# Performance work log

Measured on AMD Instinct MI355X. Metric: run time of the kernel, lower is better.

## Reference

```python
import jax, jax.numpy as jnp
import numpy as np

N, E, W_IN, W_OUT, NUM_CLASS, M = 4096, 5, 512, 128, 16, 1024
NUM_LAYERS, ALPHA, THETA = 64, 0.1, 0.5

def leaky_relu(x):
    return jnp.where(x >= 0, x, 0.01 * x)

def setup_inputs() -> dict:
    key = jax.random.key(0)
    ks = jax.random.split(key, 16)
    u = jax.random.uniform(ks[0], (N, N, E), jnp.float32)
    A = jnp.where(u < 0.01, u, 0.0)
    X = jax.random.normal(ks[1], (N, W_IN), jnp.float32)
    target_x = jax.random.randint(ks[2], (M,), 0, N)
    target = jax.random.randint(ks[3], (M,), 0, NUM_CLASS)
    def xav(k, shape):
        fan_in, fan_out = shape[-2], shape[-1]
        lim = (6.0 / (fan_in + fan_out)) ** 0.5
        return jax.random.uniform(k, shape, jnp.float32, -lim, lim)
    H0 = W_IN + E * W_OUT  # DGCN input width
    return dict(
        A=A, X=X, target_x=target_x, target=target,
        weight=xav(ks[4], (W_IN, W_OUT)),
        attw=xav(ks[5], (1, N)),
        attb=jnp.zeros((1, W_OUT), jnp.float32),
        attq=xav(ks[6], (1, W_OUT)),
        Wg=xav(ks[7], (W_IN, W_IN)), bg=jnp.zeros((W_IN,), jnp.float32),
        W0=xav(ks[8], (H0, W_OUT)), b0=jnp.zeros((W_OUT,), jnp.float32),
        Wconvs=xav(ks[9], (NUM_LAYERS, W_OUT, W_OUT)),
        Wd1=xav(ks[10], (W_OUT, W_OUT)), bd1=jnp.zeros((W_OUT,), jnp.float32),
        W1=xav(ks[11], (W_OUT, W_OUT)), b1=jnp.zeros((W_OUT,), jnp.float32),
        W2=xav(ks[12], (W_OUT, NUM_CLASS)), b2=jnp.zeros((NUM_CLASS,), jnp.float32),
    )

def reference(A, X, target_x, target, weight, attw, attb, attq, Wg, bg, W0, b0,
              Wconvs, Wd1, bd1, W1, b1, W2, b2):
    Ae = jnp.transpose(A, (2, 0, 1))              # [E,N,N]
    I = jnp.eye(N, dtype=A.dtype)
    # gcn_conv feature transform is identical for every edge type (dropout p=0)
    Xw = leaky_relu(leaky_relu(X @ Wg + bg) @ weight)   # [N, w_out]
    # norm(H, add=True): transpose, set diagonal to 1, row-normalize by degree
    Ht = Ae.transpose(0, 2, 1) * (1.0 - I) + I          # [E,N,N]
    deg = Ht.sum(-1)
    dinv = jnp.where(deg > 0, 1.0 / deg, 0.0)
    lgcn = jax.nn.relu(jnp.einsum('enm,md->end', dinv[..., None] * Ht, Xw))  # [E,N,w_out]
    # edge-type attention
    tm = jnp.tanh(jnp.einsum('n,end->ed', attw[0], lgcn) + attb)  # [E,w_out]
    watt = (tm * attq[0]).sum(-1)                                  # [E]
    beta = jax.nn.softmax(watt) * E
    Xcat = (beta[:, None, None] * lgcn).transpose(1, 0, 2).reshape(N, E * W_OUT)
    X_ = jnp.concatenate([Xcat, X], axis=1)       # [N, w_in + E*w_out]
    # DGCN: GCNII stack on binary nonzero pattern of mean adjacency, gcn_norm
    B = (jnp.mean(Ae, 0) != 0).astype(A.dtype)
    Bs = jnp.maximum(B, I)                        # add remaining self-loops
    d = Bs.sum(1)
    dis = jnp.where(d > 0, jax.lax.rsqrt(d), 0.0)
    A_hat = dis[:, None] * Bs * dis[None, :]      # D^-1/2 (B+I) D^-1/2
    x0 = jax.nn.relu(X_ @ W0 + b0)                # [N, w_out]
    betas_l = jnp.log(THETA / jnp.arange(1, NUM_LAYERS + 1, dtype=A.dtype) + 1.0)
    def step(x, inp):
        Wl, bl = inp
        h = A_hat @ x
        h = (1.0 - ALPHA) * h + ALPHA * x0        # initial residual
        x = jax.nn.relu((1.0 - bl) * h + bl * (h @ Wl))  # identity mapping
        return x, None
    x, _ = jax.lax.scan(step, x0, (Wconvs, betas_l))
    Z = leaky_relu(x @ Wd1 + bd1)                 # DGCN lins[1] + outer leaky_relu
    Z = leaky_relu(Z @ W1 + b1)                   # linear1
    y = Z[target_x] @ W2 + b2                     # linear2 on labeled nodes [M,C]
    logp = jax.nn.log_softmax(y, axis=-1)
    loss = -jnp.mean(jnp.take_along_axis(logp, target[:, None], axis=1))
    return loss, y
```

## Files before the change

### kernel.cpp

```cpp
#include <hip/hip_runtime.h>
#include <cstdint>
#include <cmath>

#define NN   4096
#define EE   5
#define WIN  512
#define WOUT 128
#define HH0  1152
#define NLAY 64
#define NCLS 16
#define MT   1024
#define GCAP 96
#define BCAP 320
#define ECAP 48
#define KSPLIT 16
#define KCHUNK 256

typedef __attribute__((ext_vector_type(8))) short     bf16x8_t;
typedef __attribute__((ext_vector_type(8))) unsigned short ushort8_t;
typedef __attribute__((ext_vector_type(4))) float     f32x4_t;

__device__ inline unsigned short f2bf(float f) {
  unsigned int u = __float_as_uint(f);
  unsigned int r = (u + 0x7FFFu + ((u >> 16) & 1u)) >> 16;
  return (unsigned short)r;
}

__device__ __forceinline__ void gload16(const unsigned short* g, unsigned short* l) {
  __builtin_amdgcn_global_load_lds(
      (__attribute__((address_space(1))) void*)g,
      (__attribute__((address_space(3))) void*)l, 16, 0, 0);
}

__global__ __launch_bounds__(256) void gemm_kernel(
    const float* __restrict__ A, const float* __restrict__ W,
    const float* __restrict__ bias, float* __restrict__ C,
    int Mdim, int Kdim, int Ndim, int act) {
  __shared__ __align__(16) float sA[16][68];
  __shared__ __align__(16) float sW[16][64];
  int tid = threadIdx.x;
  int tx = tid & 15, ty = tid >> 4;
  int row0 = blockIdx.y * 64, col0 = blockIdx.x * 64;
  float acc[4][4] = {};
  int mA = tid >> 2;
  int kA = (tid & 3) << 2;
  int kW = tid >> 4;
  int nW = (tid & 15) << 2;
  for (int k0 = 0; k0 < Kdim; k0 += 16) {
    float4 av = *(const float4*)(A + (size_t)(row0 + mA) * Kdim + k0 + kA);
    float4 wv = *(const float4*)(W + (size_t)(k0 + kW) * Ndim + col0 + nW);
    sA[kA + 0][mA] = av.x;
    sA[kA + 1][mA] = av.y;
    sA[kA + 2][mA] = av.z;
    sA[kA + 3][mA] = av.w;
    *(float4*)&sW[kW][nW] = wv;
    __syncthreads();
#pragma unroll
    for (int kk = 0; kk < 16; kk++) {
      float4 a = *(const float4*)&sA[kk][ty << 2];
      float4 b = *(const float4*)&sW[kk][tx << 2];
      acc[0][0] += a.x * b.x; acc[0][1] += a.x * b.y; acc[0][2] += a.x * b.z; acc[0][3] += a.x * b.w;
      acc[1][0] += a.y * b.x; acc[1][1] += a.y * b.y; acc[1][2] += a.y * b.z; acc[1][3] += a.y * b.w;
      acc[2][0] += a.z * b.x; acc[2][1] += a.z * b.y; acc[2][2] += a.z * b.z; acc[2][3] += a.z * b.w;
      acc[3][0] += a.w * b.x; acc[3][1] += a.w * b.y; acc[3][2] += a.w * b.z; acc[3][3] += a.w * b.w;
    }
    __syncthreads();
  }
#pragma unroll
  for (int i = 0; i < 4; i++) {
    int r = row0 + (ty << 2) + i;
#pragma unroll
    for (int jc = 0; jc < 4; jc++) {
      int c = col0 + (tx << 2) + jc;
      float o = acc[i][jc];
      if (bias) o += bias[c];
      if (act == 1) o = fmaxf(o, 0.f);
      else if (act == 2) o = (o >= 0.f) ? o : 0.01f * o;
      C[(size_t)r * Ndim + c] = o;
    }
  }
}

__global__ __launch_bounds__(256) void scan_rows_kernel(
    const float* __restrict__ A, int* __restrict__ fcnt, int* __restrict__ fidx,
    float* __restrict__ fval, int* __restrict__ bcnt, int* __restrict__ bidx) {
  __shared__ int   lbuf[1024];
  __shared__ int   lcnt;
  __shared__ int   ecnt[EE];
  __shared__ int   en2[EE][ECAP];
  __shared__ float ev[EE][ECAP];
  __shared__ int   rbase;
  __shared__ int   gbase[EE];
  int tid = threadIdx.x;
  int n1 = blockIdx.x >> 2;
  int qb = (blockIdx.x & 3) << 10;
  if (tid == 0) lcnt = 0;
  if (tid < EE) ecnt[tid] = 0;
  __syncthreads();
  const float4* src = (const float4*)(A + ((size_t)n1 * NN + qb) * EE);
  float buf[20];
  float4* bf4 = (float4*)buf;
#pragma unroll
  for (int c = 0; c < 5; c++) bf4[c] = src[tid * 5 + c];
  int n2base = qb + tid * 4;
#pragma unroll
  for (int u = 0; u < 4; u++) {
    int n2 = n2base + u;
    if (n2 == n1) continue;
    bool any = false;
#pragma unroll
    for (int e = 0; e < EE; e++) {
      float v = buf[u * 5 + e];
      if (v != 0.f) {
        any = true;
        int s = atomicAdd(&ecnt[e], 1);
        if (s < ECAP) { en2[e][s] = n2; ev[e][s] = v; }
      }
    }
    if (any) {
      int s = atomicAdd(&lcnt, 1);
      lbuf[s] = n2;
    }
  }
  __syncthreads();
  if (tid == 0) rbase = atomicAdd(&bcnt[n1], lcnt);
  if (tid < EE) gbase[tid] = atomicAdd(&fcnt[tid * NN + n1], min(ecnt[tid], ECAP));
  __syncthreads();
  int c = lcnt, rb = rbase;
  for (int s = tid; s < c; s += 256)
    if (rb + s < BCAP) bidx[(size_t)n1 * BCAP + rb + s] = lbuf[s];
#pragma unroll
  for (int e = 0; e < EE; e++) {
    int ec = min(ecnt[e], ECAP), gb = gbase[e];
    size_t base = ((size_t)e * NN + n1) * GCAP;
    for (int s = tid; s < ec; s += 256) {
      if (gb + s < GCAP) {
        fidx[base + gb + s] = en2[e][s];
        fval[base + gb + s] = ev[e][s];
      }
    }
  }
}

__global__ __launch_bounds__(64) void transpose_kernel(
    const int* __restrict__ fcnt, const int* __restrict__ fidx, const float* __restrict__ fval,
    int* __restrict__ gcnt, int* __restrict__ gidx, float* __restrict__ gval) {
  int id = blockIdx.x;
  int n1 = id & (NN - 1);
  int e  = id >> 12;
  int c = min(fcnt[id], GCAP);
  for (int s = threadIdx.x; s < c; s += 64) {
    int   n2 = fidx[(size_t)id * GCAP + s];
    float v  = fval[(size_t)id * GCAP + s];
    int t = e * NN + n2;
    int slot = atomicAdd(&gcnt[t], 1);
    if (slot < GCAP) {
      gidx[(size_t)t * GCAP + slot] = n1;
      gval[(size_t)t * GCAP + slot] = v;
    }
  }
}

__global__ void dinv_dis_kernel(const int* __restrict__ gcnt, const float* __restrict__ gval,
                                float* __restrict__ dinv, const int* __restrict__ bcnt,
                                float* __restrict__ dis) {
  int t = blockIdx.x * 256 + threadIdx.x;
  if (t < EE * NN) {
    int cnt = min(gcnt[t], GCAP);
    float s = 1.0f;
    for (int k = 0; k < cnt; k++) s += gval[(size_t)t * GCAP + k];
    dinv[t] = 1.0f / s;
  }
  if (t < NN) dis[t] = rsqrtf(1.0f + (float)min(bcnt[t], BCAP));
}

__global__ __launch_bounds__(256) void build_ahat_kernel(
    const int* __restrict__ bcnt, const int* __restrict__ bidx,
    const float* __restrict__ dis, unsigned short* __restrict__ Ab) {
  __shared__ unsigned int bits[128];
  int i = blockIdx.x, t = threadIdx.x;
  if (t < 128) bits[t] = 0;
  __syncthreads();
  int cnt = min(bcnt[i], BCAP);
  for (int s = t; s < cnt; s += 256) {
    int j = bidx[(size_t)i * BCAP + s];
    atomicOr(&bits[j >> 5], 1u << (j & 31));
  }
  __syncthreads();
  float di = dis[i];
  int c0 = t * 16;
  unsigned short out[16];
#pragma unroll
  for (int u = 0; u < 16; u++) {
    int j = c0 + u;
    bool on = ((bits[j >> 5] >> (j & 31)) & 1u) || (j == i);
    out[u] = on ? f2bf(di * dis[j]) : (unsigned short)0;
  }
  *(ushort8_t*)&Ab[(size_t)i * NN + c0]     = *(ushort8_t*)&out[0];
  *(ushort8_t*)&Ab[(size_t)i * NN + c0 + 8] = *(ushort8_t*)&out[8];
}

__global__ __launch_bounds__(128) void lgcn_kernel(
    const int* __restrict__ gcnt, const int* __restrict__ gidx, const float* __restrict__ gval,
    const float* __restrict__ dinv, const float* __restrict__ Xw, float* __restrict__ lgcn) {
  int i = blockIdx.x, e = blockIdx.y, d = threadIdx.x;
  int t = e * NN + i;
  int cnt = min(gcnt[t], GCAP);
  __shared__ int   sj[GCAP];
  __shared__ float sv[GCAP];
  for (int s = d; s < cnt; s += 128) {
    sj[s] = gidx[(size_t)t * GCAP + s];
    sv[s] = gval[(size_t)t * GCAP + s];
  }
  __syncthreads();
  float acc = Xw[(size_t)i * WOUT + d];
  for (int s = 0; s < cnt; s++) acc += sv[s] * Xw[(size_t)sj[s] * WOUT + d];
  float r = dinv[t] * acc;
  lgcn[(size_t)t * WOUT + d] = fmaxf(r, 0.f);
}

__global__ void att_partial_kernel(const float* __restrict__ lgcn, const float* __restrict__ attw,
                                   float* __restrict__ tm_pre) {
  int e = blockIdx.y, d = threadIdx.x;
  int nbase = blockIdx.x * 128;
  float acc = 0.f;
  for (int k = 0; k < 128; k++) {
    int n = nbase + k;
    acc += attw[n] * lgcn[((size_t)(e * NN + n)) * WOUT + d];
  }
  atomicAdd(&tm_pre[e * WOUT + d], acc);
}

__global__ void att_final_kernel(const float* __restrict__ tm_pre, const float* __restrict__ attb,
                                 const float* __restrict__ attq, float* __restrict__ beta) {
  int lane = threadIdx.x;
  __shared__ float sw[EE];
  for (int e = 0; e < EE; e++) {
    float v = 0.f;
    for (int d = lane; d < WOUT; d += 64) {
      float tmv = tanhf(tm_pre[e * WOUT + d] + attb[d]);
      v += tmv * attq[d];
    }
    for (int off = 32; off; off >>= 1) v += __shfl_down(v, off, 64);
    if (lane == 0) sw[e] = v;
  }
  __syncthreads();
  if (lane == 0) {
    float mx = sw[0];
    for (int e = 1; e < EE; e++) mx = fmaxf(mx, sw[e]);
    float se = 0.f, ex[EE];
    for (int e = 0; e < EE; e++) { ex[e] = expf(sw[e] - mx); se += ex[e]; }
    for (int e = 0; e < EE; e++) beta[e] = ex[e] / se * (float)EE;
  }
}

__global__ void xcat_kernel(const float* __restrict__ lgcn, const float* __restrict__ X,
                            const float* __restrict__ beta, float* __restrict__ Xc) {
  int idx = blockIdx.x * 256 + threadIdx.x;
  const int total = NN * HH0;
  for (; idx < total; idx += gridDim.x * 256) {
    int n = idx / HH0, c = idx - n * HH0;
    float v;
    if (c < EE * WOUT) {
      int e = c >> 7, d = c & 127;
      v = beta[e] * lgcn[((size_t)(e * NN + n)) * WOUT + d];
    } else {
      v = X[(size_t)n * WIN + (c - EE * WOUT)];
    }
    Xc[idx] = v;
  }
}

__global__ __launch_bounds__(256) void xT_convert_kernel(
    const float* __restrict__ x, unsigned short* __restrict__ xT) {
  __shared__ float sh2[128][36];
  int r0 = blockIdx.x * 32, t = threadIdx.x;
  const float4* x4 = (const float4*)(x + (size_t)r0 * WOUT);
#pragma unroll
  for (int q = 0; q < 4; q++) {
    int lin = t + q * 256;
    int r = lin >> 5, c = (lin & 31) * 4;
    float4 v = x4[lin];
    sh2[c + 0][r] = v.x; sh2[c + 1][r] = v.y; sh2[c + 2][r] = v.z; sh2[c + 3][r] = v.w;
  }
  __syncthreads();
  int c = t >> 1, half = t & 1;
  unsigned short tmp[16];
#pragma unroll
  for (int rr = 0; rr < 16; rr++) tmp[rr] = f2bf(sh2[c][half * 16 + rr]);
  *(ushort8_t*)&xT[(size_t)c * NN + r0 + half * 16]     = *(ushort8_t*)&tmp[0];
  *(ushort8_t*)&xT[(size_t)c * NN + r0 + half * 16 + 8] = *(ushort8_t*)&tmp[8];
}

__global__ __launch_bounds__(256) void spmm_kernel(
    const unsigned short* __restrict__ Ab, const unsigned short* __restrict__ xbT,
    float* __restrict__ P) {
  __shared__ __align__(16) unsigned short sA[128 * 32];
  __shared__ __align__(16) unsigned short sX[128 * 32];
  int t = threadIdx.x;
  int rt = blockIdx.x & 31, kc = blockIdx.x >> 5;
  int r0 = rt * 128, k0 = kc * KCHUNK;
  int wave = t >> 6, lane = t & 63;
  int wr = (wave & 1) * 64, wc = (wave >> 1) * 64;
  int quad = lane >> 4, mrow = lane & 15;
  f32x4_t acc[4][4] = {};

  int srow = wave * 32;
  int lrow = lane >> 2;
  int lk8  = (lane & 3) * 8;
  const unsigned short* gA = Ab  + (size_t)(r0 + srow + lrow) * NN + k0 + lk8;
  const unsigned short* gX = xbT + (size_t)(srow + lrow) * NN + k0 + lk8;
  unsigned short* lA = sA + srow * 32;
  unsigned short* lX = sX + srow * 32;

  for (int ks = 0; ks < KCHUNK; ks += 32) {
    gload16(gA + ks,           lA);
    gload16(gA + ks + 16 * NN, lA + 16 * 32);
    gload16(gX + ks,           lX);
    gload16(gX + ks + 16 * NN, lX + 16 * 32);
    __syncthreads();
    bf16x8_t af[4], bfv[4];
#pragma unroll
    for (int mi = 0; mi < 4; mi++)
      af[mi] = *(const bf16x8_t*)&sA[(wr + mi * 16 + mrow) * 32 + quad * 8];
#pragma unroll
    for (int nj = 0; nj < 4; nj++)
      bfv[nj] = *(const bf16x8_t*)&sX[(wc + nj * 16 + mrow) * 32 + quad * 8];
#pragma unroll
    for (int mi = 0; mi < 4; mi++)
#pragma unroll
      for (int nj = 0; nj < 4; nj++)
        acc[mi][nj] = __builtin_amdgcn_mfma_f32_16x16x32_bf16(af[mi], bfv[nj], acc[mi][nj], 0, 0, 0);
    __syncthreads();
  }

  float* Pk = P + (size_t)kc * (NN * WOUT);
#pragma unroll
  for (int mi = 0; mi < 4; mi++)
#pragma unroll
    for (int nj = 0; nj < 4; nj++) {
#pragma unroll
      for (int r4 = 0; r4 < 4; r4++) {
        int row = r0 + wr + mi * 16 + quad * 4 + r4;
        int col = wc + nj * 16 + mrow;
        Pk[(size_t)row * WOUT + col] = acc[mi][nj][r4];
      }
    }
}

__global__ __launch_bounds__(256) void gcnii_epi_kernel(
    const float* __restrict__ P, const float* __restrict__ x0,
    const float* __restrict__ Wl, float bl,
    float* __restrict__ xout_f32, unsigned short* __restrict__ xoutT, int write_f32) {
  __shared__ float sh2[128][22];
  int r0 = blockIdx.x * 16, t = threadIdx.x;
#pragma unroll
  for (int q = 0; q < 2; q++) {
    int lin = t + q * 256;
    int r = lin >> 5, c = (lin & 31) * 4;
    size_t base4 = ((size_t)(r0 + r) * WOUT + c) >> 2;
    float4 s = {0.f, 0.f, 0.f, 0.f};
#pragma unroll
    for (int kc = 0; kc < KSPLIT; kc++) {
      float4 p = ((const float4*)P)[(size_t)kc * (NN * WOUT / 4) + base4];
      s.x += p.x; s.y += p.y; s.z += p.z; s.w += p.w;
    }
    float4 xv = ((const float4*)x0)[base4];
    s.x = 0.9f * s.x + 0.1f * xv.x;
    s.y = 0.9f * s.y + 0.1f * xv.y;
    s.z = 0.9f * s.z + 0.1f * xv.z;
    s.w = 0.9f * s.w + 0.1f * xv.w;
    sh2[c + 0][r] = s.x; sh2[c + 1][r] = s.y; sh2[c + 2][r] = s.z; sh2[c + 3][r] = s.w;
  }
  __syncthreads();
  int tx = t & 31, ty = t >> 5;
  float2 hv[4];
#pragma unroll
  for (int j = 0; j < 4; j++) hv[j] = *(const float2*)&sh2[tx * 4 + j][ty * 2];
  float o[2][4] = {};
  for (int k = 0; k < WOUT; k++) {
    float2 a = *(const float2*)&sh2[k][ty * 2];
    float4 w = *(const float4*)&Wl[k * WOUT + tx * 4];
    o[0][0] += a.x * w.x; o[0][1] += a.x * w.y; o[0][2] += a.x * w.z; o[0][3] += a.x * w.w;
    o[1][0] += a.y * w.x; o[1][1] += a.y * w.y; o[1][2] += a.y * w.z; o[1][3] += a.y * w.w;
  }
  float c1 = 1.f - bl;
  float y[2][4];
  float hvv[2][4] = {{hv[0].x, hv[1].x, hv[2].x, hv[3].x},
                     {hv[0].y, hv[1].y, hv[2].y, hv[3].y}};
#pragma unroll
  for (int i = 0; i < 2; i++)
#pragma unroll
    for (int j = 0; j < 4; j++)
      y[i][j] = fmaxf(c1 * hvv[i][j] + bl * o[i][j], 0.f);
  if (write_f32) {
#pragma unroll
    for (int i = 0; i < 2; i++) {
      float4 v = {y[i][0], y[i][1], y[i][2], y[i][3]};
      *(float4*)&xout_f32[(size_t)(r0 + ty * 2 + i) * WOUT + tx * 4] = v;
    }
  }
  __syncthreads();
#pragma unroll
  for (int i = 0; i < 2; i++)
#pragma unroll
    for (int j = 0; j < 4; j++)
      sh2[tx * 4 + j][ty * 2 + i] = y[i][j];
  __syncthreads();
  int c = t >> 1, half = t & 1;
  unsigned short tmp[8];
#pragma unroll
  for (int rr = 0; rr < 8; rr++) tmp[rr] = f2bf(sh2[c][half * 8 + rr]);
  *(ushort8_t*)&xoutT[(size_t)c * NN + r0 + half * 8] = *(ushort8_t*)&tmp[0];
}

__global__ __launch_bounds__(256) void head_kernel(
    const float* __restrict__ Z, const int* __restrict__ txv, const int* __restrict__ tgt,
    const float* __restrict__ W2, const float* __restrict__ b2,
    float* __restrict__ out_y, float* __restrict__ lossp) {
  int tid = threadIdx.x;
  int mr = tid >> 4, c = tid & 15;
  int m = blockIdx.x * 16 + mr;
  const float* zr = Z + (size_t)txv[m] * WOUT;
  float acc = b2[c];
  for (int k = 0; k < WOUT; k++) acc += zr[k] * W2[k * NCLS + c];
  out_y[(size_t)m * NCLS + c] = acc;
  float mx = acc;
  for (int off = 8; off; off >>= 1) mx = fmaxf(mx, __shfl_xor(mx, off, 16));
  float ex = expf(acc - mx);
  float se = ex;
  for (int off = 8; off; off >>= 1) se += __shfl_xor(se, off, 16);
  float lse = mx + logf(se);
  float contrib = (c == tgt[m]) ? (lse - acc) : 0.f;
  __shared__ float red[256];
  red[tid] = contrib;
  __syncthreads();
  for (int stp = 128; stp; stp >>= 1) {
    if (tid < stp) red[tid] += red[tid + stp];
    __syncthreads();
  }
  if (tid == 0) lossp[blockIdx.x] = red[0];
}

__global__ void loss_final_kernel(const float* __restrict__ lossp, float* __restrict__ out_loss) {
  int lane = threadIdx.x;
  float v = (lane < 64) ? lossp[lane] : 0.f;
  for (int off = 32; off; off >>= 1) v += __shfl_down(v, off, 64);
  if (lane == 0) out_loss[0] = v / (float)MT;
}

extern "C" void kernel_launch(void* const* d_in, const int* in_sizes, int n_in,
                              void* d_out, int out_size, void* d_ws, size_t ws_size,
                              hipStream_t stream) {
  const float* A      = (const float*)d_in[0];
  const float* X      = (const float*)d_in[1];
  const int*   txv    = (const int*)d_in[2];
  const int*   tgt    = (const int*)d_in[3];
  const float* weight = (const float*)d_in[4];
  const float* attw   = (const float*)d_in[5];
  const float* attb   = (const float*)d_in[6];
  const float* attq   = (const float*)d_in[7];
  const float* Wg     = (const float*)d_in[8];
  const float* bg     = (const float*)d_in[9];
  const float* W0     = (const float*)d_in[10];
  const float* b0     = (const float*)d_in[11];
  const float* Wconvs = (const float*)d_in[12];
  const float* Wd1    = (const float*)d_in[13];
  const float* bd1    = (const float*)d_in[14];
  const float* W1     = (const float*)d_in[15];
  const float* b1     = (const float*)d_in[16];
  const float* W2     = (const float*)d_in[17];
  const float* b2     = (const float*)d_in[18];

  float* ws  = (float*)d_ws;
  int*   wsi = (int*)d_ws;

  const size_t O_GCNT  = 0;
  const size_t O_BCNT  = 20480;
  const size_t O_FCNT  = 24576;
  const size_t O_DINV  = 45056;
  const size_t O_DIS   = 65536;
  const size_t O_TMPRE = 69632;
  const size_t O_BETA  = 70272;
  const size_t O_LOSSP = 70288;
  const size_t O_GIDX  = 71680;
  const size_t O_GVAL  = O_GIDX + 1966080;
  const size_t O_FIDX  = O_GVAL + 1966080;
  const size_t O_FVAL  = O_FIDX + 1966080;
  const size_t O_BIDX  = O_FVAL + 1966080;
  const size_t O_LGCN  = O_BIDX + 1310720;
  const size_t O_XW    = O_LGCN + 2621440;
  const size_t O_X0    = O_XW   + 524288;
  const size_t O_XA    = O_X0   + 524288;
  const size_t O_XB    = O_XA   + 524288;
  const size_t O_AB    = O_XB   + 524288;
  const size_t O_XBT0  = O_AB   + 8388608;
  const size_t O_XBT1  = O_XBT0 + 262144;
  const size_t O_P     = O_XBT1 + 262144;
  const size_t O_T1    = O_FVAL;
  const size_t O_XCAT  = O_GIDX;

  hipMemsetAsync(ws + O_GCNT, 0, 45056 * 4, stream);
  hipMemsetAsync(ws + O_TMPRE, 0, 640 * 4, stream);

  dim3 blk(256);
  gemm_kernel<<<dim3(WIN / 64, NN / 64), blk, 0, stream>>>(X, Wg, bg, ws + O_T1, NN, WIN, WIN, 2);
  gemm_kernel<<<dim3(WOUT / 64, NN / 64), blk, 0, stream>>>(ws + O_T1, weight, nullptr, ws + O_XW, NN, WIN, WOUT, 2);
  scan_rows_kernel<<<NN * 4, 256, 0, stream>>>(A, wsi + O_FCNT, wsi + O_FIDX, ws + O_FVAL,
                                               wsi + O_BCNT, wsi + O_BIDX);
  transpose_kernel<<<EE * NN, 64, 0, stream>>>(wsi + O_FCNT, wsi + O_FIDX, ws + O_FVAL,
                                               wsi + O_GCNT, wsi + O_GIDX, ws + O_GVAL);
  dinv_dis_kernel<<<80, 256, 0, stream>>>(wsi + O_GCNT, ws + O_GVAL, ws + O_DINV,
                                          wsi + O_BCNT, ws + O_DIS);
  build_ahat_kernel<<<NN, 256, 0, stream>>>(wsi + O_BCNT, wsi + O_BIDX, ws + O_DIS,
                                            (unsigned short*)(ws + O_AB));
  lgcn_kernel<<<dim3(NN, EE), 128, 0, stream>>>(wsi + O_GCNT, wsi + O_GIDX, ws + O_GVAL,
                                                ws + O_DINV, ws + O_XW, ws + O_LGCN);
  att_partial_kernel<<<dim3(32, EE), 128, 0, stream>>>(ws + O_LGCN, attw, ws + O_TMPRE);
  att_final_kernel<<<1, 64, 0, stream>>>(ws + O_TMPRE, attb, attq, ws + O_BETA);
  xcat_kernel<<<4096, 256, 0, stream>>>(ws + O_LGCN, X, ws + O_BETA, ws + O_XCAT);
  gemm_kernel<<<dim3(WOUT / 64, NN / 64), blk, 0, stream>>>(ws + O_XCAT, W0, b0, ws + O_X0, NN, HH0, WOUT, 1);
  xT_convert_kernel<<<NN / 32, 256, 0, stream>>>(ws + O_X0, (unsigned short*)(ws + O_XBT0));
  for (int l = 0; l < NLAY; l++) {
    float bl = logf(0.5f / (float)(l + 1) + 1.0f);
    const unsigned short* xin = (const unsigned short*)(ws + ((l & 1) ? O_XBT1 : O_XBT0));
    unsigned short* xoT = (unsigned short*)(ws + ((l & 1) ? O_XBT0 : O_XBT1));
    spmm_kernel<<<32 * KSPLIT, 256, 0, stream>>>((const unsigned short*)(ws + O_AB), xin, ws + O_P);
    gcnii_epi_kernel<<<NN / 16, 256, 0, stream>>>(ws + O_P, ws + O_X0,
                                                  Wconvs + (size_t)l * WOUT * WOUT, bl,
                                                  ws + O_XA, xoT, (l == NLAY - 1) ? 1 : 0);
  }
  gemm_kernel<<<dim3(WOUT / 64, NN / 64), blk, 0, stream>>>(ws + O_XA, Wd1, bd1, ws + O_XB, NN, WOUT, WOUT, 2);
  gemm_kernel<<<dim3(WOUT / 64, NN / 64), blk, 0, stream>>>(ws + O_XB, W1, b1, ws + O_X0, NN, WOUT, WOUT, 2);
  head_kernel<<<MT / 16, 256, 0, stream>>>(ws + O_X0, txv, tgt, W2, b2,
                                           (float*)d_out + 1, ws + O_LOSSP);
  loss_final_kernel<<<1, 64, 0, stream>>>(ws + O_LOSSP, (float*)d_out);
}
```

Measured before the change: 2.682 ms.

## Double-buffer LDS tiles in spmm kernel to overlap global loads with MFMA

The spmm kernel now keeps two LDS buffers. Each stage loads a 64-wide K slice split into two 32-wide subtiles. The load for the next stage is issued before the MFMA work on the current buffer, and a single vmcnt wait plus barrier at the end of each stage replaces the two __syncthreads per 32-wide step. The goal is to hide global-to-LDS latency behind matrix math and cut barrier count. The cost is four times the LDS footprint, which may lower occupancy, and more live registers for the fragments.

```diff
diff --git a/kernel.cpp b/kernel.cpp
--- a/kernel.cpp
+++ b/kernel.cpp
@@ -292,11 +292,12 @@
   *(ushort8_t*)&xT[(size_t)c * NN + r0 + half * 16 + 8] = *(ushort8_t*)&tmp[8];
 }
 
+#define SUBSZ (128 * 32)
 __global__ __launch_bounds__(256) void spmm_kernel(
     const unsigned short* __restrict__ Ab, const unsigned short* __restrict__ xbT,
     float* __restrict__ P) {
-  __shared__ __align__(16) unsigned short sA[128 * 32];
-  __shared__ __align__(16) unsigned short sX[128 * 32];
+  __shared__ __align__(16) unsigned short sAx[2][2][SUBSZ];
+  __shared__ __align__(16) unsigned short sXx[2][2][SUBSZ];
   int t = threadIdx.x;
   int rt = blockIdx.x & 31, kc = blockIdx.x >> 5;
   int r0 = rt * 128, k0 = kc * KCHUNK;
@@ -306,33 +307,55 @@
   f32x4_t acc[4][4] = {};
 
   int srow = wave * 32;
-  int lrow = lane >> 2;
-  int lk8  = (lane & 3) * 8;
-  const unsigned short* gA = Ab  + (size_t)(r0 + srow + lrow) * NN + k0 + lk8;
-  const unsigned short* gX = xbT + (size_t)(srow + lrow) * NN + k0 + lk8;
-  unsigned short* lA = sA + srow * 32;
-  unsigned short* lX = sX + srow * 32;
-
-  for (int ks = 0; ks < KCHUNK; ks += 32) {
-    gload16(gA + ks,           lA);
-    gload16(gA + ks + 16 * NN, lA + 16 * 32);
-    gload16(gX + ks,           lX);
-    gload16(gX + ks + 16 * NN, lX + 16 * 32);
-    __syncthreads();
-    bf16x8_t af[4], bfv[4];
-#pragma unroll
-    for (int mi = 0; mi < 4; mi++)
-      af[mi] = *(const bf16x8_t*)&sA[(wr + mi * 16 + mrow) * 32 + quad * 8];
-#pragma unroll
-    for (int nj = 0; nj < 4; nj++)
-      bfv[nj] = *(const bf16x8_t*)&sX[(wc + nj * 16 + mrow) * 32 + quad * 8];
-#pragma unroll
-    for (int mi = 0; mi < 4; mi++)
+  const unsigned short* gA = Ab  + (size_t)(r0 + srow + (lane >> 2)) * NN + k0 + (lane & 3) * 8;
+  const unsigned short* gX = xbT + (size_t)(srow + (lane >> 2)) * NN + k0 + (lane & 3) * 8;
+
+#define STAGE(BUF, KS)                                                          \
+  {                                                                             \
+    unsigned short* la = &sAx[(BUF)][0][srow * 32];                             \
+    unsigned short* lx = &sXx[(BUF)][0][srow * 32];                             \
+    _Pragma("unroll")                                                           \
+    for (int s = 0; s < 2; s++) {                                               \
+      _Pragma("unroll")                                                         \
+      for (int h = 0; h < 2; h++) {                                             \
+        gload16(gA + (KS) + s * 32 + h * 16 * NN, la + s * SUBSZ + h * 16 * 32);\
+        gload16(gX + (KS) + s * 32 + h * 16 * NN, lx + s * SUBSZ + h * 16 * 32);\
+      }                                                                         \
+    }                                                                           \
+  }
+
+  STAGE(0, 0);
+  asm volatile("s_waitcnt vmcnt(0)" ::: "memory");
+  __builtin_amdgcn_s_barrier();
+
+  int cur = 0;
+#pragma unroll
+  for (int tt = 0; tt < 4; tt++) {
+    if (tt < 3) STAGE(cur ^ 1, (tt + 1) * 64);
+    bf16x8_t af[2][4], bfv[2][4];
+#pragma unroll
+    for (int kk = 0; kk < 2; kk++) {
+#pragma unroll
+      for (int mi = 0; mi < 4; mi++)
+        af[kk][mi] = *(const bf16x8_t*)&sAx[cur][kk][(wr + mi * 16 + mrow) * 32 + quad * 8];
 #pragma unroll
       for (int nj = 0; nj < 4; nj++)
-        acc[mi][nj] = __builtin_amdgcn_mfma_f32_16x16x32_bf16(af[mi], bfv[nj], acc[mi][nj], 0, 0, 0);
-    __syncthreads();
-  }
+        bfv[kk][nj] = *(const bf16x8_t*)&sXx[cur][kk][(wc + nj * 16 + mrow) * 32 + quad * 8];
+    }
+#pragma unroll
+    for (int kk = 0; kk < 2; kk++)
+#pragma unroll
+      for (int mi = 0; mi < 4; mi++)
+#pragma unroll
+        for (int nj = 0; nj < 4; nj++)
+          acc[mi][nj] = __builtin_amdgcn_mfma_f32_16x16x32_bf16(af[kk][mi], bfv[kk][nj], acc[mi][nj], 0, 0, 0);
+    if (tt < 3) {
+      asm volatile("s_waitcnt vmcnt(0)" ::: "memory");
+      __builtin_amdgcn_s_barrier();
+      cur ^= 1;
+    }
+  }
+#undef STAGE
 
   float* Pk = P + (size_t)kc * (NN * WOUT);
 #pragma unroll
```

New measurement: 2.663 ms. Within noise of the previous version (-0.7%).

## Fuse dense A_hat propagation with GCNII epilogue in one kernel per layer

Applied to the files above, without the earlier changes.

Replaces the split-K spmm kernel plus separate epilogue kernel with one fused kernel per layer. Each block owns 16 rows, walks the full K=4096 with double-buffered LDS tiles via direct global-to-LDS loads, and applies the residual, Wl matmul, ReLU and bf16 transpose in place. This removes the 16-way partial-sum buffer write/read and one launch per layer. In exchange each block re-reads the whole x^T (1 MB) for only 16 rows, the K loop is long and serial, and each wave does just two MFMAs per barrier.

```diff
diff --git a/kernel.cpp b/kernel.cpp
--- a/kernel.cpp
+++ b/kernel.cpp
@@ -13,8 +13,6 @@
 #define GCAP 96
 #define BCAP 320
 #define ECAP 48
-#define KSPLIT 16
-#define KCHUNK 256
 
 typedef __attribute__((ext_vector_type(8))) short     bf16x8_t;
 typedef __attribute__((ext_vector_type(8))) unsigned short ushort8_t;
@@ -292,126 +290,113 @@
   *(ushort8_t*)&xT[(size_t)c * NN + r0 + half * 16 + 8] = *(ushort8_t*)&tmp[8];
 }
 
-__global__ __launch_bounds__(256) void spmm_kernel(
+__global__ __launch_bounds__(512) void gcnii_fused_kernel(
     const unsigned short* __restrict__ Ab, const unsigned short* __restrict__ xbT,
-    float* __restrict__ P) {
-  __shared__ __align__(16) unsigned short sA[128 * 32];
-  __shared__ __align__(16) unsigned short sX[128 * 32];
+    const float* __restrict__ x0, const float* __restrict__ Wl, float bl,
+    float* __restrict__ xout_f32, unsigned short* __restrict__ xoutT, int write_f32) {
+  __shared__ __align__(16) unsigned short sT[2][9216];
+  __shared__ float sh2[128][22];
   int t = threadIdx.x;
-  int rt = blockIdx.x & 31, kc = blockIdx.x >> 5;
-  int r0 = rt * 128, k0 = kc * KCHUNK;
   int wave = t >> 6, lane = t & 63;
-  int wr = (wave & 1) * 64, wc = (wave >> 1) * 64;
+  int r0 = blockIdx.x * 16;
+  int wc = wave * 16;
   int quad = lane >> 4, mrow = lane & 15;
-  f32x4_t acc[4][4] = {};
-
-  int srow = wave * 32;
-  int lrow = lane >> 2;
-  int lk8  = (lane & 3) * 8;
-  const unsigned short* gA = Ab  + (size_t)(r0 + srow + lrow) * NN + k0 + lk8;
-  const unsigned short* gX = xbT + (size_t)(srow + lrow) * NN + k0 + lk8;
-  unsigned short* lA = sA + srow * 32;
-  unsigned short* lX = sX + srow * 32;
-
-  for (int ks = 0; ks < KCHUNK; ks += 32) {
-    gload16(gA + ks,           lA);
-    gload16(gA + ks + 16 * NN, lA + 16 * 32);
-    gload16(gX + ks,           lX);
-    gload16(gX + ks + 16 * NN, lX + 16 * 32);
-    __syncthreads();
-    bf16x8_t af[4], bfv[4];
-#pragma unroll
-    for (int mi = 0; mi < 4; mi++)
-      af[mi] = *(const bf16x8_t*)&sA[(wr + mi * 16 + mrow) * 32 + quad * 8];
-#pragma unroll
-    for (int nj = 0; nj < 4; nj++)
-      bfv[nj] = *(const bf16x8_t*)&sX[(wc + nj * 16 + mrow) * 32 + quad * 8];
-#pragma unroll
-    for (int mi = 0; mi < 4; mi++)
-#pragma unroll
-      for (int nj = 0; nj < 4; nj++)
-        acc[mi][nj] = __builtin_amdgcn_mfma_f32_16x16x32_bf16(af[mi], bfv[nj], acc[mi][nj], 0, 0, 0);
-    __syncthreads();
-  }
-
-  float* Pk = P + (size_t)kc * (NN * WOUT);
-#pragma unroll
-  for (int mi = 0; mi < 4; mi++)
-#pragma unroll
-    for (int nj = 0; nj < 4; nj++) {
-#pragma unroll
-      for (int r4 = 0; r4 < 4; r4++) {
-        int row = r0 + wr + mi * 16 + quad * 4 + r4;
-        int col = wc + nj * 16 + mrow;
-        Pk[(size_t)row * WOUT + col] = acc[mi][nj][r4];
-      }
-    }
-}
-
-__global__ __launch_bounds__(256) void gcnii_epi_kernel(
-    const float* __restrict__ P, const float* __restrict__ x0,
-    const float* __restrict__ Wl, float bl,
-    float* __restrict__ xout_f32, unsigned short* __restrict__ xoutT, int write_f32) {
-  __shared__ float sh2[128][22];
-  int r0 = blockIdx.x * 16, t = threadIdx.x;
-#pragma unroll
-  for (int q = 0; q < 2; q++) {
-    int lin = t + q * 256;
-    int r = lin >> 5, c = (lin & 31) * 4;
-    size_t base4 = ((size_t)(r0 + r) * WOUT + c) >> 2;
-    float4 s = {0.f, 0.f, 0.f, 0.f};
-#pragma unroll
-    for (int kc = 0; kc < KSPLIT; kc++) {
-      float4 p = ((const float4*)P)[(size_t)kc * (NN * WOUT / 4) + base4];
-      s.x += p.x; s.y += p.y; s.z += p.z; s.w += p.w;
-    }
-    float4 xv = ((const float4*)x0)[base4];
-    s.x = 0.9f * s.x + 0.1f * xv.x;
-    s.y = 0.9f * s.y + 0.1f * xv.y;
-    s.z = 0.9f * s.z + 0.1f * xv.z;
-    s.w = 0.9f * s.w + 0.1f * xv.w;
-    sh2[c + 0][r] = s.x; sh2[c + 1][r] = s.y; sh2[c + 2][r] = s.z; sh2[c + 3][r] = s.w;
-  }
-  __syncthreads();
-  int tx = t & 31, ty = t >> 5;
-  float2 hv[4];
-#pragma unroll
-  for (int j = 0; j < 4; j++) hv[j] = *(const float2*)&sh2[tx * 4 + j][ty * 2];
-  float o[2][4] = {};
+  f32x4_t acc = {0.f, 0.f, 0.f, 0.f};
+
+  const unsigned short* gq[3];
+  int lq[3];
+#pragma unroll
+  for (int q = 0; q < 3; q++) {
+    int c = wave + q * 8;
+    if (c < 2) {
+      gq[q] = Ab + (size_t)(r0 + (lane >> 2)) * NN + c * 32 + (lane & 3) * 8;
+      lq[q] = c * 512;
+    } else if (c < 18) {
+      int cc = c - 2;
+      int sub = cc >> 3, rb = cc & 7;
+      gq[q] = xbT + (size_t)(rb * 16 + (lane >> 2)) * NN + sub * 32 + (lane & 3) * 8;
+      lq[q] = 1024 + sub * 4096 + rb * 512;
+    } else {
+      gq[q] = Ab;
+      lq[q] = 0;
+    }
+  }
+  int nq3 = (wave < 2) ? 1 : 0;
+
+#define STAGE(BUF, TS)                                           \
+  {                                                              \
+    unsigned short* lb = &sT[(BUF)][0];                          \
+    gload16(gq[0] + (size_t)(TS) * 64, lb + lq[0]);              \
+    gload16(gq[1] + (size_t)(TS) * 64, lb + lq[1]);              \
+    if (nq3) gload16(gq[2] + (size_t)(TS) * 64, lb + lq[2]);     \
+  }
+
+  STAGE(0, 0);
+  asm volatile("s_waitcnt vmcnt(0)" ::: "memory");
+  __builtin_amdgcn_s_barrier();
+
+  int cur = 0;
+  for (int tt = 0; tt < 64; tt++) {
+    if (tt < 63) STAGE(cur ^ 1, tt + 1);
+    const unsigned short* base = &sT[cur][0];
+    bf16x8_t af0 = *(const bf16x8_t*)&base[mrow * 32 + quad * 8];
+    bf16x8_t af1 = *(const bf16x8_t*)&base[512 + mrow * 32 + quad * 8];
+    bf16x8_t bf0 = *(const bf16x8_t*)&base[1024 + (wc + mrow) * 32 + quad * 8];
+    bf16x8_t bf1 = *(const bf16x8_t*)&base[1024 + 4096 + (wc + mrow) * 32 + quad * 8];
+    acc = __builtin_amdgcn_mfma_f32_16x16x32_bf16(af0, bf0, acc, 0, 0, 0);
+    acc = __builtin_amdgcn_mfma_f32_16x16x32_bf16(af1, bf1, acc, 0, 0, 0);
+    if (tt < 63) {
+      asm volatile("s_waitcnt vmcnt(0)" ::: "memory");
+      __builtin_amdgcn_s_barrier();
+      cur ^= 1;
+    }
+  }
+#undef STAGE
+
+#pragma unroll
+  for (int r4 = 0; r4 < 4; r4++) {
+    int row = quad * 4 + r4;
+    float xv = x0[(size_t)(r0 + row) * WOUT + wc + mrow];
+    sh2[wc + mrow][row] = 0.9f * acc[r4] + 0.1f * xv;
+  }
+  __syncthreads();
+  int tx2 = t & 31, ty2 = t >> 5;
+  float o0 = 0.f, o1 = 0.f, o2 = 0.f, o3 = 0.f;
+  const float* wp = Wl + tx2 * 4;
   for (int k = 0; k < WOUT; k++) {
-    float2 a = *(const float2*)&sh2[k][ty * 2];
-    float4 w = *(const float4*)&Wl[k * WOUT + tx * 4];
-    o[0][0] += a.x * w.x; o[0][1] += a.x * w.y; o[0][2] += a.x * w.z; o[0][3] += a.x * w.w;
-    o[1][0] += a.y * w.x; o[1][1] += a.y * w.y; o[1][2] += a.y * w.z; o[1][3] += a.y * w.w;
+    float aa = sh2[k][ty2];
+    float4 w = *(const float4*)(wp + k * WOUT);
+    o0 = fmaf(aa, w.x, o0);
+    o1 = fmaf(aa, w.y, o1);
+    o2 = fmaf(aa, w.z, o2);
+    o3 = fmaf(aa, w.w, o3);
   }
   float c1 = 1.f - bl;
-  float y[2][4];
-  float hvv[2][4] = {{hv[0].x, hv[1].x, hv[2].x, hv[3].x},
-                     {hv[0].y, hv[1].y, hv[2].y, hv[3].y}};
-#pragma unroll
-  for (int i = 0; i < 2; i++)
-#pragma unroll
-    for (int j = 0; j < 4; j++)
-      y[i][j] = fmaxf(c1 * hvv[i][j] + bl * o[i][j], 0.f);
+  float h0 = sh2[tx2 * 4 + 0][ty2];
+  float h1 = sh2[tx2 * 4 + 1][ty2];
+  float h2 = sh2[tx2 * 4 + 2][ty2];
+  float h3 = sh2[tx2 * 4 + 3][ty2];
+  float y0 = fmaxf(c1 * h0 + bl * o0, 0.f);
+  float y1 = fmaxf(c1 * h1 + bl * o1, 0.f);
+  float y2 = fmaxf(c1 * h2 + bl * o2, 0.f);
+  float y3 = fmaxf(c1 * h3 + bl * o3, 0.f);
   if (write_f32) {
-#pragma unroll
-    for (int i = 0; i < 2; i++) {
-      float4 v = {y[i][0], y[i][1], y[i][2], y[i][3]};
-      *(float4*)&xout_f32[(size_t)(r0 + ty * 2 + i) * WOUT + tx * 4] = v;
-    }
-  }
-  __syncthreads();
-#pragma unroll
-  for (int i = 0; i < 2; i++)
-#pragma unroll
-    for (int j = 0; j < 4; j++)
-      sh2[tx * 4 + j][ty * 2 + i] = y[i][j];
-  __syncthreads();
-  int c = t >> 1, half = t & 1;
-  unsigned short tmp[8];
-#pragma unroll
-  for (int rr = 0; rr < 8; rr++) tmp[rr] = f2bf(sh2[c][half * 8 + rr]);
-  *(ushort8_t*)&xoutT[(size_t)c * NN + r0 + half * 8] = *(ushort8_t*)&tmp[0];
+    float4 v = {y0, y1, y2, y3};
+    *(float4*)&xout_f32[(size_t)(r0 + ty2) * WOUT + tx2 * 4] = v;
+  }
+  __syncthreads();
+  sh2[tx2 * 4 + 0][ty2] = y0;
+  sh2[tx2 * 4 + 1][ty2] = y1;
+  sh2[tx2 * 4 + 2][ty2] = y2;
+  sh2[tx2 * 4 + 3][ty2] = y3;
+  __syncthreads();
+  if (t < 256) {
+    int cc = t >> 1, half = t & 1;
+    unsigned short tmp[8];
+#pragma unroll
+    for (int rr = 0; rr < 8; rr++) tmp[rr] = f2bf(sh2[cc][half * 8 + rr]);
+    *(ushort8_t*)&xoutT[(size_t)cc * NN + r0 + half * 8] = *(ushort8_t*)&tmp[0];
+  }
 }
 
 __global__ __launch_bounds__(256) void head_kernel(
@@ -496,7 +481,6 @@
   const size_t O_AB    = O_XB   + 524288;
   const size_t O_XBT0  = O_AB   + 8388608;
   const size_t O_XBT1  = O_XBT0 + 262144;
-  const size_t O_P     = O_XBT1 + 262144;
   const size_t O_T1    = O_FVAL;
   const size_t O_XCAT  = O_GIDX;
 
@@ -525,10 +509,10 @@
     float bl = logf(0.5f / (float)(l + 1) + 1.0f);
     const unsigned short* xin = (const unsigned short*)(ws + ((l & 1) ? O_XBT1 : O_XBT0));
     unsigned short* xoT = (unsigned short*)(ws + ((l & 1) ? O_XBT0 : O_XBT1));
-    spmm_kernel<<<32 * KSPLIT, 256, 0, stream>>>((const unsigned short*)(ws + O_AB), xin, ws + O_P);
-    gcnii_epi_kernel<<<NN / 16, 256, 0, stream>>>(ws + O_P, ws + O_X0,
-                                                  Wconvs + (size_t)l * WOUT * WOUT, bl,
-                                                  ws + O_XA, xoT, (l == NLAY - 1) ? 1 : 0);
+    gcnii_fused_kernel<<<NN / 16, 512, 0, stream>>>(
+        (const unsigned short*)(ws + O_AB), xin, ws + O_X0,
+        Wconvs + (size_t)l * WOUT * WOUT, bl,
+        ws + O_XA, xoT, (l == NLAY - 1) ? 1 : 0);
   }
   gemm_kernel<<<dim3(WOUT / 64, NN / 64), blk, 0, stream>>>(ws + O_XA, Wd1, bd1, ws + O_XB, NN, WOUT, WOUT, 2);
   gemm_kernel<<<dim3(WOUT / 64, NN / 64), blk, 0, stream>>>(ws + O_XB, W1, b1, ws + O_X0, NN, WOUT, WOUT, 2);
```

Result: slower. 3.505 ms (+30.7%).
